# Kernel tuning notes

Measured on AMD Instinct MI355X. Metric: run time of the kernel, lower is better.

The kernel has to match this reference:

```python
import jax, jax.numpy as jnp
import numpy as np

N = 100000   # nodes
E = 1600000  # edges (avg degree 16)
F_IN, F_HID, F_OUT = 64, 64, 16


def setup_inputs() -> dict:
    key = jax.random.key(0)
    ks = jax.random.split(key, 10)
    features = jax.random.normal(ks[0], (N, F_IN), dtype=jnp.float32)
    src = jax.random.randint(ks[1], (E,), 0, N, dtype=jnp.int32)
    dst = jax.random.randint(ks[2], (E,), 0, N, dtype=jnp.int32)
    # Xavier-uniform weights, zero bias (matches nn.init in the module)
    def xavier(k, fan_in, fan_out):
        lim = np.sqrt(6.0 / (fan_in + fan_out))
        return jax.random.uniform(k, (fan_in, fan_out), jnp.float32, -lim, lim)
    return {
        "features": features,
        "W1": xavier(ks[3], F_IN, F_HID), "b1": jnp.zeros((F_HID,), jnp.float32),
        "W2": xavier(ks[4], F_HID, F_HID), "b2": jnp.zeros((F_HID,), jnp.float32),
        "W3": xavier(ks[5], F_HID, F_OUT), "b3": jnp.zeros((F_OUT,), jnp.float32),
        "src": src, "dst": dst,
    }


def pairnorm_scs(x):
    # PairNorm 'PN-SCS', scale=1
    col_mean = x.mean(axis=0)                                    # [F]
    rownorm = jnp.sqrt(1e-6 + jnp.sum(x * x, axis=1, keepdims=True))  # [N,1]
    return x / rownorm - col_mean


def graph_conv(h, src, dst, W, b):
    # copy_u('h','m') + sum reduce over edges, plus self-loop
    agg = jax.ops.segment_sum(h[src], dst, num_segments=N) + h   # [N,F]
    return agg @ W + b


def reference(features, W1, b1, W2, b2, W3, b3, src, dst):
    h = features
    for W, b in ((W1, b1), (W2, b2)):
        h = pairnorm_scs(h)
        h = jax.nn.relu(graph_conv(h, src, dst, W, b))
        # dropout p=0.0 -> identity
    return graph_conv(h, src, dst, W3, b3)
```

## Files before the change

### kernel.cpp

```cpp
#include <hip/hip_runtime.h>
#include <hip/hip_fp8.h>


#define NHB 128

__device__ __forceinline__ unsigned short f2bf(float f) {
  unsigned u = __builtin_bit_cast(unsigned, f);
  u += 0x7FFFu + ((u >> 16) & 1u);
  return (unsigned short)(u >> 16);
}
__device__ __forceinline__ float bf2f(unsigned short h) {
  return __builtin_bit_cast(float, ((unsigned)h) << 16);
}
__device__ __forceinline__ float rlane(float v, int k) {
  return __builtin_bit_cast(
      float, __builtin_amdgcn_readlane(__builtin_bit_cast(int, v), k));
}
__device__ __forceinline__ unsigned char f2fp8(float f) {
  __hip_fp8_e4m3 t(f);
  return (unsigned char)t.__x;
}
__device__ __forceinline__ float fp8tof(unsigned v) {
#if __has_builtin(__builtin_amdgcn_cvt_f32_fp8)
  return __builtin_amdgcn_cvt_f32_fp8((int)v, 0);
#else
  const unsigned h = ((v << 8) & 0x8000u) | ((v << 7) & 0x3f80u);
  __half_raw hr; hr.x = (unsigned short)h;
  return (float)__half(hr) * 256.0f;
#endif
}

__global__ __launch_bounds__(256) void prelude_kernel(
    const int* __restrict__ dst, int* __restrict__ cntA, int E,
    const float* __restrict__ x, float* __restrict__ cs, int n4) {
  __shared__ int lc[NHB];
  __shared__ float lds[16][64];
  const int t = threadIdx.x;
  if (t < NHB) lc[t] = 0;
  __syncthreads();
  const int stride = gridDim.x * blockDim.x;
  for (int e = blockIdx.x * blockDim.x + t; e < E; e += stride)
    atomicAdd(&lc[__builtin_nontemporal_load(&dst[e]) >> 10], 1);

  float s0 = 0.f, s1 = 0.f, s2 = 0.f, s3 = 0.f;
  for (int i = blockIdx.x * blockDim.x + t; i < n4; i += stride) {
    float4 v = ((const float4*)x)[i];
    s0 += v.x; s1 += v.y; s2 += v.z; s3 += v.w;
  }
  const int r = t >> 4;
  const int cq = (t & 15) * 4;
  lds[r][cq + 0] = s0; lds[r][cq + 1] = s1; lds[r][cq + 2] = s2; lds[r][cq + 3] = s3;
  __syncthreads();
  if (t < NHB && lc[t]) atomicAdd(&cntA[t], lc[t]);
  if (t < 64) {
    float tot = 0.f;
    #pragma unroll
    for (int rr = 0; rr < 16; ++rr) tot += lds[rr][t];
    unsafeAtomicAdd(&cs[t], tot);
  }
}

__global__ __launch_bounds__(256) void matnorm_kernel(
    const float* x, const float* __restrict__ W,
    const float* __restrict__ cs, unsigned char* __restrict__ z,
    int N, float invN) {
  const int lane = threadIdx.x & 63;
  const int wid  = blockIdx.x * (blockDim.x >> 6) + (threadIdx.x >> 6);
  const int nw   = gridDim.x * (blockDim.x >> 6);

  float w[64];
  float cm0 = 0.f, cm1 = 0.f, cm2 = 0.f, cm3 = 0.f;
  #pragma unroll
  for (int k = 0; k < 64; k += 4) {
    w[k + 0] = W[(k + 0) * 64 + lane];
    w[k + 1] = W[(k + 1) * 64 + lane];
    w[k + 2] = W[(k + 2) * 64 + lane];
    w[k + 3] = W[(k + 3) * 64 + lane];
    cm0 = fmaf(cs[k + 0], w[k + 0], cm0);
    cm1 = fmaf(cs[k + 1], w[k + 1], cm1);
    cm2 = fmaf(cs[k + 2], w[k + 2], cm2);
    cm3 = fmaf(cs[k + 3], w[k + 3], cm3);
  }
  const float cm = ((cm0 + cm1) + (cm2 + cm3)) * invN;

  for (int row = wid; row < N; row += nw) {
    const float xv = x[(size_t)row * 64 + lane];
    float ss = xv * xv;
    #pragma unroll
    for (int m = 1; m < 64; m <<= 1) ss += __shfl_xor(ss, m, 64);
    const float rinv = 1.0f / sqrtf(1e-6f + ss);
    float a0 = 0.f, a1 = 0.f, a2 = 0.f, a3 = 0.f;
    #pragma unroll
    for (int k = 0; k < 64; k += 4) {
      a0 = fmaf(rlane(xv, k + 0), w[k + 0], a0);
      a1 = fmaf(rlane(xv, k + 1), w[k + 1], a1);
      a2 = fmaf(rlane(xv, k + 2), w[k + 2], a2);
      a3 = fmaf(rlane(xv, k + 3), w[k + 3], a3);
    }
    const float acc = (a0 + a1) + (a2 + a3);
    z[(size_t)row * 64 + lane] = f2fp8(acc * rinv - cm);
  }
}


__global__ void scanA_kernel(const int* __restrict__ cntA,
                             int* __restrict__ baseA, int* __restrict__ curA,
                             int NHI) {
  __shared__ int s[NHB];
  const int t = threadIdx.x;
  const int v = (t < NHI) ? cntA[t] : 0;
  s[t] = v;
  __syncthreads();
  int acc = v;
  for (int off = 1; off < NHB; off <<= 1) {
    const int add = (t >= off) ? s[t - off] : 0;
    __syncthreads();
    acc += add;
    s[t] = acc;
    __syncthreads();
  }
  const int excl = acc - v;
  if (t < NHI) { baseA[t] = excl; curA[t] = excl; }
  if (t == NHI - 1) baseA[NHI] = acc;
}

#define TILE 2048
#define CAPA 48
__global__ __launch_bounds__(256) void scatterA_kernel(
    const int* __restrict__ src, const int* __restrict__ dst,
    int* __restrict__ curA, unsigned* __restrict__ ppack, int E) {
  __shared__ unsigned lpk[NHB][CAPA];
  __shared__ int lcnt[NHB], lbase[NHB];
  const int t = threadIdx.x;
  if (t < NHB) lcnt[t] = 0;
  __syncthreads();
  const int ntiles = (E + TILE - 1) / TILE;
  for (int tile = blockIdx.x; tile < ntiles; tile += gridDim.x) {
    const int base = tile * TILE;
    #pragma unroll
    for (int j = 0; j < TILE / 256; ++j) {
      const int e = base + j * 256 + t;
      if (e < E) {
        const int d = __builtin_nontemporal_load(&dst[e]);
        const int s = __builtin_nontemporal_load(&src[e]);
        const unsigned pw = ((unsigned)s << 10) | ((unsigned)d & 1023u);
        const int p = d >> 10;
        const int slot = atomicAdd(&lcnt[p], 1);
        if (slot < CAPA) lpk[p][slot] = pw;
        else ppack[atomicAdd(&curA[p], 1)] = pw;
      }
    }
    __syncthreads();
    if (t < NHB) {
      int c = lcnt[t]; if (c > CAPA) c = CAPA;
      lbase[t] = c ? atomicAdd(&curA[t], c) : 0;
      lcnt[t] = c;
    }
    __syncthreads();
    for (int p = 0; p < NHB; ++p) {
      const int c = lcnt[p];
      if (t < c) ppack[lbase[p] + t] = lpk[p][t];
    }
    __syncthreads();
    if (t < NHB) lcnt[t] = 0;
    __syncthreads();
  }
}

__global__ __launch_bounds__(1024) void fillsort_kernel(
    const unsigned* __restrict__ ppack, const int* __restrict__ baseA,
    int* __restrict__ rowstart, int* __restrict__ csr, int N, int E) {
  __shared__ int hist[1024];
  __shared__ int bs[1024];
  const int t = threadIdx.x;
  const int h = blockIdx.x;
  const int nlo = h << 10;
  const int elo = baseA[h], ehi = baseA[h + 1];

  hist[t] = 0;
  __syncthreads();

  int e = elo + t;
  for (; e + 3 * 1024 < ehi; e += 4 * 1024) {
    const unsigned p0 = ppack[e], p1 = ppack[e + 1024],
                   p2 = ppack[e + 2048], p3 = ppack[e + 3072];
    atomicAdd(&hist[p0 & 1023u], 1); atomicAdd(&hist[p1 & 1023u], 1);
    atomicAdd(&hist[p2 & 1023u], 1); atomicAdd(&hist[p3 & 1023u], 1);
  }
  for (; e < ehi; e += 1024) atomicAdd(&hist[ppack[e] & 1023u], 1);
  __syncthreads();

  const int c = hist[t];
  bs[t] = c;
  __syncthreads();
  for (int off = 1; off < 1024; off <<= 1) {
    const int v = (t >= off) ? bs[t - off] : 0;
    __syncthreads();
    bs[t] += v;
    __syncthreads();
  }
  const int excl = bs[t] - c;

  hist[t] = excl;
  const int n0 = nlo + t;
  if (n0 < N) rowstart[n0] = elo + excl;
  if (h == 0 && t == 0) rowstart[N] = E;
  __syncthreads();

  e = elo + t;
  for (; e + 3 * 1024 < ehi; e += 4 * 1024) {
    const unsigned p0 = ppack[e],        p1 = ppack[e + 1024];
    const unsigned p2 = ppack[e + 2048], p3 = ppack[e + 3072];
    csr[elo + atomicAdd(&hist[p0 & 1023u], 1)] = (int)(p0 >> 10);
    csr[elo + atomicAdd(&hist[p1 & 1023u], 1)] = (int)(p1 >> 10);
    csr[elo + atomicAdd(&hist[p2 & 1023u], 1)] = (int)(p2 >> 10);
    csr[elo + atomicAdd(&hist[p3 & 1023u], 1)] = (int)(p3 >> 10);
  }
  for (; e < ehi; e += 1024) {
    const unsigned p = ppack[e];
    csr[elo + atomicAdd(&hist[p & 1023u], 1)] = (int)(p >> 10);
  }
}

__global__ __launch_bounds__(256) void gather64_kernel(
    const unsigned char* __restrict__ z, const float* __restrict__ b,
    const int* __restrict__ rowstart, const int* __restrict__ csr,
    float* __restrict__ agg, float* __restrict__ cs, int N) {
  __shared__ float lred[4][64];
  const int lane = threadIdx.x & 63;
  const int wv   = threadIdx.x >> 6;
  const int nw   = gridDim.x * (blockDim.x >> 6);
  const float bl = b[lane];
  float csum = 0.f;
  for (int node = blockIdx.x * (blockDim.x >> 6) + wv; node < N; node += nw) {
    const int n = __builtin_amdgcn_readfirstlane(node);
    const int start = rowstart[n];
    const int end   = rowstart[n + 1];
    const unsigned char hs = z[(size_t)n * 64 + lane];
    float a0 = 0.f, a1 = 0.f, a2 = 0.f, a3 = 0.f;
    int e = start;
    for (; e + 16 <= end; e += 16) {
      unsigned char h[16];
      #pragma unroll
      for (int j = 0; j < 16; ++j) h[j] = z[(size_t)csr[e + j] * 64 + lane];
      #pragma unroll
      for (int j = 0; j < 16; j += 4) {
        a0 += fp8tof(h[j + 0]); a1 += fp8tof(h[j + 1]);
        a2 += fp8tof(h[j + 2]); a3 += fp8tof(h[j + 3]);
      }
    }
    for (; e + 4 <= end; e += 4) {
      unsigned char h[4];
      #pragma unroll
      for (int j = 0; j < 4; ++j) h[j] = z[(size_t)csr[e + j] * 64 + lane];
      a0 += fp8tof(h[0]); a1 += fp8tof(h[1]); a2 += fp8tof(h[2]); a3 += fp8tof(h[3]);
    }
    for (; e < end; ++e) a0 += fp8tof(z[(size_t)csr[e] * 64 + lane]);
    const float sum = (a0 + a1) + (a2 + a3);
    const float o = fmaxf(fp8tof(hs) + bl + sum, 0.f);
    agg[(size_t)n * 64 + lane] = o;
    csum += o;
  }
  lred[wv][lane] = csum;
  __syncthreads();
  if (threadIdx.x < 64) {
    const float tot = lred[0][lane] + lred[1][lane] + lred[2][lane] + lred[3][lane];
    unsafeAtomicAdd(&cs[lane], tot);
  }
}

__global__ __launch_bounds__(256) void gather_l2_kernel(
    const unsigned char* __restrict__ z2, const float* __restrict__ b2,
    const float* __restrict__ W3, const int* __restrict__ rowstart,
    const int* __restrict__ csr, unsigned char* __restrict__ z3, int N) {
  const int lane = threadIdx.x & 63;
  int node = blockIdx.x * (blockDim.x >> 6) + (threadIdx.x >> 6);
  if (node >= N) return;
  node = __builtin_amdgcn_readfirstlane(node);
  float4 w4[4];
  #pragma unroll
  for (int q = 0; q < 4; ++q)
    w4[q] = ((const float4*)(W3 + lane * 16))[q];

  const int start = rowstart[node];
  const int end   = rowstart[node + 1];
  const unsigned char hs = z2[(size_t)node * 64 + lane];
  float a0 = 0.f, a1 = 0.f, a2 = 0.f, a3 = 0.f;
  int e = start;
  for (; e + 16 <= end; e += 16) {
    unsigned char h[16];
    #pragma unroll
    for (int j = 0; j < 16; ++j) h[j] = z2[(size_t)csr[e + j] * 64 + lane];
    #pragma unroll
    for (int j = 0; j < 16; j += 4) {
      a0 += fp8tof(h[j + 0]); a1 += fp8tof(h[j + 1]);
      a2 += fp8tof(h[j + 2]); a3 += fp8tof(h[j + 3]);
    }
  }
  for (; e + 4 <= end; e += 4) {
    unsigned char h[4];
    #pragma unroll
    for (int j = 0; j < 4; ++j) h[j] = z2[(size_t)csr[e + j] * 64 + lane];
    a0 += fp8tof(h[0]); a1 += fp8tof(h[1]); a2 += fp8tof(h[2]); a3 += fp8tof(h[3]);
  }
  for (; e < end; ++e) a0 += fp8tof(z2[(size_t)csr[e] * 64 + lane]);
  const float sum = (a0 + a1) + (a2 + a3);
  const float o = fmaxf(fp8tof(hs) + b2[lane] + sum, 0.f);

  float p[16];
  #pragma unroll
  for (int q = 0; q < 4; ++q) {
    p[4 * q + 0] = o * w4[q].x;
    p[4 * q + 1] = o * w4[q].y;
    p[4 * q + 2] = o * w4[q].z;
    p[4 * q + 3] = o * w4[q].w;
  }
  {
    const bool up = (lane & 1);
    #pragma unroll
    for (int m = 0; m < 8; ++m) {
      const float mine = up ? p[m + 8] : p[m];
      const float give = up ? p[m] : p[m + 8];
      p[m] = mine + __shfl_xor(give, 1, 64);
    }
  }
  {
    const bool up = (lane & 2);
    #pragma unroll
    for (int m = 0; m < 4; ++m) {
      const float mine = up ? p[m + 4] : p[m];
      const float give = up ? p[m] : p[m + 4];
      p[m] = mine + __shfl_xor(give, 2, 64);
    }
  }
  {
    const bool up = (lane & 4);
    #pragma unroll
    for (int m = 0; m < 2; ++m) {
      const float mine = up ? p[m + 2] : p[m];
      const float give = up ? p[m] : p[m + 2];
      p[m] = mine + __shfl_xor(give, 4, 64);
    }
  }
  {
    const bool up = (lane & 8);
    const float mine = up ? p[1] : p[0];
    const float give = up ? p[0] : p[1];
    p[0] = mine + __shfl_xor(give, 8, 64);
  }
  p[0] += __shfl_xor(p[0], 16, 64);
  p[0] += __shfl_xor(p[0], 32, 64);

  if (lane < 16) {
    const int j = ((lane & 1) << 3) | ((lane & 2) << 1) |
                  ((lane & 4) >> 1) | ((lane & 8) >> 3);
    z3[(size_t)node * 16 + j] = f2fp8(p[0]);
  }
}

__global__ __launch_bounds__(256) void gather16_kernel(
    const unsigned char* __restrict__ z3, const float* __restrict__ b3,
    const int* __restrict__ rowstart, const int* __restrict__ csr,
    float* __restrict__ out, int N) {
  const int lane = threadIdx.x & 63;
  const int f = lane & 15;
  const int g = lane >> 4;
  int node = blockIdx.x * (blockDim.x >> 6) + (threadIdx.x >> 6);
  if (node >= N) return;
  node = __builtin_amdgcn_readfirstlane(node);
  const int start = rowstart[node];
  const int end   = rowstart[node + 1];
  float acc0 = 0.f, acc1 = 0.f;
  int e = start + g;
  for (; e + 4 < end; e += 8) {
    acc0 += fp8tof(z3[(size_t)csr[e] * 16 + f]);
    acc1 += fp8tof(z3[(size_t)csr[e + 4] * 16 + f]);
  }
  if (e < end) acc0 += fp8tof(z3[(size_t)csr[e] * 16 + f]);
  float acc = acc0 + acc1;
  acc += __shfl_xor(acc, 16, 64);
  acc += __shfl_xor(acc, 32, 64);
  if (lane < 16)
    out[(size_t)node * 16 + f] = fp8tof(z3[(size_t)node * 16 + f]) + b3[f] + acc;
}

extern "C" void kernel_launch(void* const* d_in, const int* in_sizes, int n_in,
                              void* d_out, int out_size, void* d_ws, size_t ws_size,
                              hipStream_t stream) {
  const float* feat = (const float*)d_in[0];
  const float* W1 = (const float*)d_in[1];
  const float* b1 = (const float*)d_in[2];
  const float* W2 = (const float*)d_in[3];
  const float* b2 = (const float*)d_in[4];
  const float* W3 = (const float*)d_in[5];
  const float* b3 = (const float*)d_in[6];
  const int* src = (const int*)d_in[7];
  const int* dst = (const int*)d_in[8];
  const int N = in_sizes[0] / 64;
  const int E = in_sizes[7];
  float* out = (float*)d_out;

  float* B            = (float*)d_ws;
  unsigned char* zb   = (unsigned char*)(B + (size_t)N * 64);
  unsigned char* z3b  = zb + (size_t)N * 64;
  int* cntA  = (int*)(z3b + (size_t)N * 16);
  float* cs1 = (float*)(cntA + NHB);
  float* cs2 = cs1 + 64;
  int* baseA    = (int*)(cs2 + 64);
  int* curA     = baseA + NHB + 1;
  int* rowstart = curA + NHB;
  int* csr      = rowstart + N + 1;
  unsigned* ppack = (unsigned*)zb;

  const int NHI = (N + 1023) >> 10;
  const int node_blocks = (N + 3) / 4;
  const float invN = 1.0f / (float)N;

  hipMemsetAsync(cntA, 0, (NHB + 128) * sizeof(int), stream);
  prelude_kernel<<<512, 256, 0, stream>>>(dst, cntA, E, feat, cs1, N * 16);
  scanA_kernel<<<1, NHB, 0, stream>>>(cntA, baseA, curA, NHI);
  scatterA_kernel<<<512, 256, 0, stream>>>(src, dst, curA, ppack, E);
  fillsort_kernel<<<NHI, 1024, 0, stream>>>(ppack, baseA, rowstart, csr, N, E);

  matnorm_kernel<<<1024, 256, 0, stream>>>(feat, W1, cs1, zb, N, invN);
  gather64_kernel<<<2048, 256, 0, stream>>>(zb, b1, rowstart, csr, B, cs2, N);

  matnorm_kernel<<<1024, 256, 0, stream>>>(B, W2, cs2, zb, N, invN);
  gather_l2_kernel<<<node_blocks, 256, 0, stream>>>(zb, b2, W3, rowstart, csr,
                                                    z3b, N);

  gather16_kernel<<<node_blocks, 256, 0, stream>>>(z3b, b3, rowstart, csr, out, N);
}
```

Measured before the change: 401.5 us.

## Defer layer-2 column-mean subtraction to the gather via a degree-scaled correction

The layer-2 PairNorm column mean is no longer accumulated in the layer-1 gather. The matnorm2 kernel computes the column sums while it projects, and a tiny kernel forms cm·W2. The layer-2 gather subtracts (deg+1)·(cm·W2) after aggregation, using linearity. This lets gather64 become a simple one-node-per-wave kernel without the strided loop or atomics. It adds one small launch, and quantising the un-centred values to fp8 may change the accuracy.

```diff
diff --git a/kernel.cpp b/kernel.cpp
--- a/kernel.cpp
+++ b/kernel.cpp
@@ -102,6 +102,66 @@
   }
 }
 
+__global__ __launch_bounds__(256) void matnorm2_kernel(
+    const float* x, const float* __restrict__ W,
+    float* __restrict__ cs, unsigned char* __restrict__ z, int N) {
+  __shared__ float lred[4][64];
+  const int lane = threadIdx.x & 63;
+  const int wv   = threadIdx.x >> 6;
+  const int wid  = blockIdx.x * (blockDim.x >> 6) + wv;
+  const int nw   = gridDim.x * (blockDim.x >> 6);
+
+  float w[64];
+  #pragma unroll
+  for (int k = 0; k < 64; k += 4) {
+    w[k + 0] = W[(k + 0) * 64 + lane];
+    w[k + 1] = W[(k + 1) * 64 + lane];
+    w[k + 2] = W[(k + 2) * 64 + lane];
+    w[k + 3] = W[(k + 3) * 64 + lane];
+  }
+
+  float csum = 0.f;
+  for (int row = wid; row < N; row += nw) {
+    const float xv = x[(size_t)row * 64 + lane];
+    csum += xv;
+    float ss = xv * xv;
+    #pragma unroll
+    for (int m = 1; m < 64; m <<= 1) ss += __shfl_xor(ss, m, 64);
+    const float rinv = 1.0f / sqrtf(1e-6f + ss);
+    float a0 = 0.f, a1 = 0.f, a2 = 0.f, a3 = 0.f;
+    #pragma unroll
+    for (int k = 0; k < 64; k += 4) {
+      a0 = fmaf(rlane(xv, k + 0), w[k + 0], a0);
+      a1 = fmaf(rlane(xv, k + 1), w[k + 1], a1);
+      a2 = fmaf(rlane(xv, k + 2), w[k + 2], a2);
+      a3 = fmaf(rlane(xv, k + 3), w[k + 3], a3);
+    }
+    const float acc = (a0 + a1) + (a2 + a3);
+    z[(size_t)row * 64 + lane] = f2fp8(acc * rinv);
+  }
+  lred[wv][lane] = csum;
+  __syncthreads();
+  if (threadIdx.x < 64) {
+    const float tot = lred[0][lane] + lred[1][lane] + lred[2][lane] + lred[3][lane];
+    unsafeAtomicAdd(&cs[lane], tot);
+  }
+}
+
+__global__ void cm2_kernel(const float* __restrict__ cs,
+                           const float* __restrict__ W,
+                           float* __restrict__ cm2, float invN) {
+  const int m = threadIdx.x;
+  float a0 = 0.f, a1 = 0.f, a2 = 0.f, a3 = 0.f;
+  #pragma unroll
+  for (int k = 0; k < 64; k += 4) {
+    a0 = fmaf(cs[k + 0], W[(k + 0) * 64 + m], a0);
+    a1 = fmaf(cs[k + 1], W[(k + 1) * 64 + m], a1);
+    a2 = fmaf(cs[k + 2], W[(k + 2) * 64 + m], a2);
+    a3 = fmaf(cs[k + 3], W[(k + 3) * 64 + m], a3);
+  }
+  cm2[m] = ((a0 + a1) + (a2 + a3)) * invN;
+}
+
 
 __global__ void scanA_kernel(const int* __restrict__ cntA,
                              int* __restrict__ baseA, int* __restrict__ curA,
@@ -225,54 +285,42 @@
 __global__ __launch_bounds__(256) void gather64_kernel(
     const unsigned char* __restrict__ z, const float* __restrict__ b,
     const int* __restrict__ rowstart, const int* __restrict__ csr,
-    float* __restrict__ agg, float* __restrict__ cs, int N) {
-  __shared__ float lred[4][64];
+    float* __restrict__ agg, int N) {
   const int lane = threadIdx.x & 63;
-  const int wv   = threadIdx.x >> 6;
-  const int nw   = gridDim.x * (blockDim.x >> 6);
-  const float bl = b[lane];
-  float csum = 0.f;
-  for (int node = blockIdx.x * (blockDim.x >> 6) + wv; node < N; node += nw) {
-    const int n = __builtin_amdgcn_readfirstlane(node);
-    const int start = rowstart[n];
-    const int end   = rowstart[n + 1];
-    const unsigned char hs = z[(size_t)n * 64 + lane];
-    float a0 = 0.f, a1 = 0.f, a2 = 0.f, a3 = 0.f;
-    int e = start;
-    for (; e + 16 <= end; e += 16) {
-      unsigned char h[16];
-      #pragma unroll
-      for (int j = 0; j < 16; ++j) h[j] = z[(size_t)csr[e + j] * 64 + lane];
-      #pragma unroll
-      for (int j = 0; j < 16; j += 4) {
-        a0 += fp8tof(h[j + 0]); a1 += fp8tof(h[j + 1]);
-        a2 += fp8tof(h[j + 2]); a3 += fp8tof(h[j + 3]);
-      }
-    }
-    for (; e + 4 <= end; e += 4) {
-      unsigned char h[4];
-      #pragma unroll
-      for (int j = 0; j < 4; ++j) h[j] = z[(size_t)csr[e + j] * 64 + lane];
-      a0 += fp8tof(h[0]); a1 += fp8tof(h[1]); a2 += fp8tof(h[2]); a3 += fp8tof(h[3]);
-    }
-    for (; e < end; ++e) a0 += fp8tof(z[(size_t)csr[e] * 64 + lane]);
-    const float sum = (a0 + a1) + (a2 + a3);
-    const float o = fmaxf(fp8tof(hs) + bl + sum, 0.f);
-    agg[(size_t)n * 64 + lane] = o;
-    csum += o;
-  }
-  lred[wv][lane] = csum;
-  __syncthreads();
-  if (threadIdx.x < 64) {
-    const float tot = lred[0][lane] + lred[1][lane] + lred[2][lane] + lred[3][lane];
-    unsafeAtomicAdd(&cs[lane], tot);
-  }
+  int node = blockIdx.x * (blockDim.x >> 6) + (threadIdx.x >> 6);
+  if (node >= N) return;
+  node = __builtin_amdgcn_readfirstlane(node);
+  const int start = rowstart[node];
+  const int end   = rowstart[node + 1];
+  const unsigned char hs = z[(size_t)node * 64 + lane];
+  float a0 = 0.f, a1 = 0.f, a2 = 0.f, a3 = 0.f;
+  int e = start;
+  for (; e + 16 <= end; e += 16) {
+    unsigned char h[16];
+    #pragma unroll
+    for (int j = 0; j < 16; ++j) h[j] = z[(size_t)csr[e + j] * 64 + lane];
+    #pragma unroll
+    for (int j = 0; j < 16; j += 4) {
+      a0 += fp8tof(h[j + 0]); a1 += fp8tof(h[j + 1]);
+      a2 += fp8tof(h[j + 2]); a3 += fp8tof(h[j + 3]);
+    }
+  }
+  for (; e + 4 <= end; e += 4) {
+    unsigned char h[4];
+    #pragma unroll
+    for (int j = 0; j < 4; ++j) h[j] = z[(size_t)csr[e + j] * 64 + lane];
+    a0 += fp8tof(h[0]); a1 += fp8tof(h[1]); a2 += fp8tof(h[2]); a3 += fp8tof(h[3]);
+  }
+  for (; e < end; ++e) a0 += fp8tof(z[(size_t)csr[e] * 64 + lane]);
+  const float sum = (a0 + a1) + (a2 + a3);
+  agg[(size_t)node * 64 + lane] = fmaxf(fp8tof(hs) + b[lane] + sum, 0.f);
 }
 
 __global__ __launch_bounds__(256) void gather_l2_kernel(
     const unsigned char* __restrict__ z2, const float* __restrict__ b2,
-    const float* __restrict__ W3, const int* __restrict__ rowstart,
-    const int* __restrict__ csr, unsigned char* __restrict__ z3, int N) {
+    const float* __restrict__ W3, const float* __restrict__ cm2,
+    const int* __restrict__ rowstart, const int* __restrict__ csr,
+    unsigned char* __restrict__ z3, int N) {
   const int lane = threadIdx.x & 63;
   int node = blockIdx.x * (blockDim.x >> 6) + (threadIdx.x >> 6);
   if (node >= N) return;
@@ -281,6 +329,7 @@
   #pragma unroll
   for (int q = 0; q < 4; ++q)
     w4[q] = ((const float4*)(W3 + lane * 16))[q];
+  const float cml = cm2[lane];
 
   const int start = rowstart[node];
   const int end   = rowstart[node + 1];
@@ -305,7 +354,8 @@
   }
   for (; e < end; ++e) a0 += fp8tof(z2[(size_t)csr[e] * 64 + lane]);
   const float sum = (a0 + a1) + (a2 + a3);
-  const float o = fmaxf(fp8tof(hs) + b2[lane] + sum, 0.f);
+  const float corr = (float)(end - start + 1) * cml;
+  const float o = fmaxf(fp8tof(hs) + b2[lane] + sum - corr, 0.f);
 
   float p[16];
   #pragma unroll
@@ -406,7 +456,8 @@
   int* cntA  = (int*)(z3b + (size_t)N * 16);
   float* cs1 = (float*)(cntA + NHB);
   float* cs2 = cs1 + 64;
-  int* baseA    = (int*)(cs2 + 64);
+  float* cm2w = cs2 + 64;
+  int* baseA    = (int*)(cm2w + 64);
   int* curA     = baseA + NHB + 1;
   int* rowstart = curA + NHB;
   int* csr      = rowstart + N + 1;
@@ -423,11 +474,12 @@
   fillsort_kernel<<<NHI, 1024, 0, stream>>>(ppack, baseA, rowstart, csr, N, E);
 
   matnorm_kernel<<<1024, 256, 0, stream>>>(feat, W1, cs1, zb, N, invN);
-  gather64_kernel<<<2048, 256, 0, stream>>>(zb, b1, rowstart, csr, B, cs2, N);
-
-  matnorm_kernel<<<1024, 256, 0, stream>>>(B, W2, cs2, zb, N, invN);
-  gather_l2_kernel<<<node_blocks, 256, 0, stream>>>(zb, b2, W3, rowstart, csr,
-                                                    z3b, N);
+  gather64_kernel<<<node_blocks, 256, 0, stream>>>(zb, b1, rowstart, csr, B, N);
+
+  matnorm2_kernel<<<1024, 256, 0, stream>>>(B, W2, cs2, zb, N);
+  cm2_kernel<<<1, 64, 0, stream>>>(cs2, W2, cm2w, invN);
+  gather_l2_kernel<<<node_blocks, 256, 0, stream>>>(zb, b2, W3, cm2w, rowstart,
+                                                    csr, z3b, N);
 
   gather16_kernel<<<node_blocks, 256, 0, stream>>>(z3b, b3, rowstart, csr, out, N);
 }
```

Measured after the change: 386.9 us. -3.6%, faster.
